# Optimization experiments

Hardware: AMD Instinct MI355X
Metric: run time of the kernel (lower is better)

Reference implementation:

```python
import jax, jax.numpy as jnp
import numpy as np

B, N, E = 32, 4096, 65536          # batch, num_agents(nodes), edges per graph
DS, ES, ENC, H, OUT = 8, 4, 8, 16, 4  # node state, edge state, encoding, hidden, out_state
NI = N * DS                        # flat obs size for critic


def setup_inputs() -> dict:
    key = jax.random.key(0)
    ks = jax.random.split(key, 18)
    g = lambda k, s: jax.random.normal(k, s, dtype=jnp.float32) * 0.1
    return {
        "agent_obs": jax.random.normal(ks[0], (B, N, DS), dtype=jnp.float32),
        "edge_attr": jax.random.normal(ks[1], (B, E, ES), dtype=jnp.float32),
        "obs_flat": jax.random.normal(ks[2], (B, NI), dtype=jnp.float32),
        "edge_index": jax.random.randint(ks[3], (B, 2, E), 0, N, dtype=jnp.int64),
        "W_ne1": g(ks[4], (DS, H)), "b_ne1": g(ks[5], (H,)),
        "W_ne2": g(ks[6], (H, ENC)), "b_ne2": g(ks[7], (ENC,)),
        "W_ee": g(ks[8], (ES, ENC)), "b_ee": g(ks[9], (ENC,)),
        "W_a1": g(ks[10], (ENC, H)), "b_a1": g(ks[11], (H,)),
        "W_a2": g(ks[12], (H, OUT)), "b_a2": g(ks[13], (OUT,)),
        "W_c1": g(ks[14], (NI, H)), "b_c1": g(ks[15], (H,)),
        "W_c2": g(ks[16], (H, 1)), "b_c2": g(ks[17], (1,)),
    }


def reference(agent_obs, edge_attr, obs_flat, edge_index,
              W_ne1, b_ne1, W_ne2, b_ne2, W_ee, b_ee,
              W_a1, b_a1, W_a2, b_a2, W_c1, b_c1, W_c2, b_c2):
    # node encoder: [B,N,DS] -> [B,N,ENC]
    x = jax.nn.relu(agent_obs @ W_ne1 + b_ne1) @ W_ne2 + b_ne2
    # edge encoder: [B,E,ES] -> [B,E,ENC]
    ea = edge_attr @ W_ee + b_ee
    src = edge_index[:, 0, :]  # [B,E] message source (x_j)
    dst = edge_index[:, 1, :]  # [B,E] aggregation target (x_i)
    # GINEConv message: relu(x_j + edge_attr)
    xj = jnp.take_along_axis(x, src[..., None], axis=1)  # [B,E,ENC]
    msgs = jax.nn.relu(xj + ea)
    # sum-aggregate to targets (batched via segment offsets)
    seg = (dst + jnp.arange(B, dtype=dst.dtype)[:, None] * N).reshape(-1)
    agg = jax.ops.segment_sum(msgs.reshape(B * E, ENC), seg, num_segments=B * N)
    agg = agg.reshape(B, N, ENC)
    # GINEConv nn (eps=0): MLP((1+eps)*x + agg)
    h = jax.nn.relu((x + agg) @ W_a1 + b_a1) @ W_a2 + b_a2  # [B,N,OUT]
    # per-sample flatten, drop first agent's out slots
    outs = h.reshape(B, N * OUT)[:, OUT:]  # [B,(N-1)*OUT]
    # critic on flat obs
    values = jax.nn.relu(obs_flat @ W_c1 + b_c1) @ W_c2 + b_c2  # [B,1]
    return jnp.concatenate([outs, values], axis=-1)  # [B,(N-1)*OUT+1]
```

## Files before the change

### kernel.cpp

```cpp
#include <hip/hip_runtime.h>
#include <hip/hip_fp16.h>

#define BB 32
#define NN 4096
#define EE 65536
#define DS 8
#define ES 4
#define ENC 8
#define HH 16
#define OUTC 4
#define NI (NN * DS)
#define ROW (NN * OUTC - OUTC + 1)
#define CSPLIT 16
#define CCHUNK (NI / CSPLIT)
#define ESPLIT 8
#define EPB (EE / ESPLIT)

typedef __fp16 half2_t __attribute__((ext_vector_type(2)));

__global__ __launch_bounds__(256) void k_fusedA(
    const float* __restrict__ obs,
    const float* __restrict__ Wne1, const float* __restrict__ bne1,
    const float* __restrict__ Wne2, const float* __restrict__ bne2,
    const float* __restrict__ obsf, const float* __restrict__ Wc1,
    float* __restrict__ x, float* __restrict__ hpart) {
  __shared__ float sW1[DS * HH], sb1[HH], sW2[HH * ENC], sb2[ENC];
  __shared__ float red[4][HH];
  int t = threadIdx.x;

  if (blockIdx.x < 512) {
    if (t < DS * HH)  sW1[t] = Wne1[t];
    if (t < HH)       sb1[t] = bne1[t];
    if (t < HH * ENC) sW2[t] = Wne2[t];
    if (t < ENC)      sb2[t] = bne2[t];
    __syncthreads();
    int gid = blockIdx.x * 256 + t;

    const float4* op = (const float4*)(obs + (size_t)gid * DS);
    float4 o0 = op[0], o1 = op[1];
    float o[DS] = {o0.x, o0.y, o0.z, o0.w, o1.x, o1.y, o1.z, o1.w};

    float hb[HH];
#pragma unroll
    for (int j = 0; j < HH; ++j) {
      float a = sb1[j];
#pragma unroll
      for (int i = 0; i < DS; ++i) a += o[i] * sW1[i * HH + j];
      hb[j] = fmaxf(a, 0.f);
    }
    float e[ENC];
#pragma unroll
    for (int c = 0; c < ENC; ++c) {
      float a = sb2[c];
#pragma unroll
      for (int j = 0; j < HH; ++j) a += hb[j] * sW2[j * ENC + c];
      e[c] = a;
    }
    float4* xp = (float4*)(x + (size_t)gid * ENC);
    xp[0] = make_float4(e[0], e[1], e[2], e[3]);
    xp[1] = make_float4(e[4], e[5], e[6], e[7]);
  } else {
    int cb = blockIdx.x - 512;
    int b = cb / CSPLIT, s = cb % CSPLIT;
    float acc[HH];
#pragma unroll
    for (int j = 0; j < HH; ++j) acc[j] = 0.f;

    const float* ob = obsf + (size_t)b * NI;
    int i0 = s * CCHUNK;
    for (int i = i0 + t; i < i0 + CCHUNK; i += 256) {
      float v = ob[i];
      const float4* wr = (const float4*)(Wc1 + (size_t)i * HH);
      float4 w0 = wr[0], w1 = wr[1], w2 = wr[2], w3 = wr[3];
      acc[0]  += v * w0.x; acc[1]  += v * w0.y; acc[2]  += v * w0.z; acc[3]  += v * w0.w;
      acc[4]  += v * w1.x; acc[5]  += v * w1.y; acc[6]  += v * w1.z; acc[7]  += v * w1.w;
      acc[8]  += v * w2.x; acc[9]  += v * w2.y; acc[10] += v * w2.z; acc[11] += v * w2.w;
      acc[12] += v * w3.x; acc[13] += v * w3.y; acc[14] += v * w3.z; acc[15] += v * w3.w;
    }
    int wid = t >> 6, lane = t & 63;
#pragma unroll
    for (int j = 0; j < HH; ++j) {
      float a = acc[j];
#pragma unroll
      for (int off = 32; off >= 1; off >>= 1) a += __shfl_down(a, off, 64);
      if (lane == 0) red[wid][j] = a;
    }
    __syncthreads();
    if (t < HH)
      hpart[(size_t)cb * HH + t] = red[0][t] + red[1][t] + red[2][t] + red[3][t];
  }
}

__global__ __launch_bounds__(1024, 4) void k_edge_full(
    const float* __restrict__ eattr,
    const int* __restrict__ eidx,
    const float* __restrict__ Wee, const float* __restrict__ bee,
    const float* __restrict__ x,
    float* __restrict__ partial) {
  __shared__ uint32_t sagg[4 * NN];
  int p = blockIdx.x;
  int L = (p & 7) * 32 + (p >> 3);
  int b = L >> 3, s = L & 7;
  int t = threadIdx.x;

  float wv[ES * ENC], bv[ENC];
#pragma unroll
  for (int i = 0; i < ES * ENC; ++i) wv[i] = Wee[i];
#pragma unroll
  for (int c = 0; c < ENC; ++c) bv[c] = bee[c];

  {
    uint4 z = make_uint4(0u, 0u, 0u, 0u);
    uint4* sz = (uint4*)sagg;
#pragma unroll
    for (int i = 0; i < (4 * NN / 4) / 1024; ++i) sz[t + i * 1024] = z;
  }
  __syncthreads();

  const int*    ibs = eidx + (size_t)b * 2 * EE + (size_t)s * EPB;
  const int*    ibd = ibs + EE;
  const float4* ab4 = (const float4*)eattr + (size_t)b * EE + (size_t)s * EPB;
  const float4* xb4 = (const float4*)(x + (size_t)b * NN * ENC);

#pragma unroll
  for (int uo = 0; uo < EPB / 4096; ++uo) {
    int k = t + uo * 4096;
    int s_[4], d_[4];
    float4 a_[4];
#pragma unroll
    for (int u = 0; u < 4; ++u) { s_[u] = ibs[k + u * 1024]; d_[u] = ibd[k + u * 1024]; }
#pragma unroll
    for (int u = 0; u < 4; ++u) a_[u] = ab4[k + u * 1024];
    float4 xl[4], xh[4];
#pragma unroll
    for (int u = 0; u < 4; ++u) { xl[u] = xb4[2 * s_[u]]; xh[u] = xb4[2 * s_[u] + 1]; }
#pragma unroll
    for (int u = 0; u < 4; ++u) {
      float av[ES] = {a_[u].x, a_[u].y, a_[u].z, a_[u].w};
      float xv[ENC] = {xl[u].x, xl[u].y, xl[u].z, xl[u].w,
                       xh[u].x, xh[u].y, xh[u].z, xh[u].w};
      float m[ENC];
#pragma unroll
      for (int c = 0; c < ENC; ++c) {
        float ea = bv[c];
#pragma unroll
        for (int i2 = 0; i2 < ES; ++i2) ea += av[i2] * wv[i2 * ENC + c];
        m[c] = fmaxf(xv[c] + ea, 0.f);
      }
      uint32_t base = (uint32_t)(uintptr_t)(&sagg[d_[u]]);
#pragma unroll
      for (int cp = 0; cp < 4; ++cp) {
        half2_t pk = __builtin_amdgcn_cvt_pkrtz(m[2 * cp], m[2 * cp + 1]);
        uint32_t pku = __builtin_bit_cast(uint32_t, pk);
        uint32_t addr = base + (uint32_t)(cp * NN * 4);
        asm volatile("ds_pk_add_f16 %0, %1" :: "v"(addr), "v"(pku) : "memory");
      }
    }
  }
  __syncthreads();

  float* pb = partial + (size_t)L * NN * ENC;
#pragma unroll
  for (int i = 0; i < NN / 1024; ++i) {
    int n = t + i * 1024;
    uint32_t w0 = sagg[0 * NN + n], w1 = sagg[1 * NN + n];
    uint32_t w2 = sagg[2 * NN + n], w3 = sagg[3 * NN + n];
    half2_t h0 = __builtin_bit_cast(half2_t, w0);
    half2_t h1 = __builtin_bit_cast(half2_t, w1);
    half2_t h2 = __builtin_bit_cast(half2_t, w2);
    half2_t h3 = __builtin_bit_cast(half2_t, w3);
    float4 lo = make_float4((float)h0[0], (float)h0[1], (float)h1[0], (float)h1[1]);
    float4 hi = make_float4((float)h2[0], (float)h2[1], (float)h3[0], (float)h3[1]);
    float4* dp = (float4*)(pb + (size_t)n * ENC);
    dp[0] = lo; dp[1] = hi;
  }
}

__global__ __launch_bounds__(256) void k_fusedC(
    const float* __restrict__ x, const float* __restrict__ partial,
    const float* __restrict__ Wa1, const float* __restrict__ ba1,
    const float* __restrict__ Wa2, const float* __restrict__ ba2,
    const float* __restrict__ hpart,
    const float* __restrict__ bc1,
    const float* __restrict__ Wc2, const float* __restrict__ bc2,
    float* __restrict__ out) {
  int t = threadIdx.x;
  if (blockIdx.x == 512) {
    if (t < BB) {
      int b = t;
      float val = bc2[0];
#pragma unroll
      for (int j = 0; j < HH; ++j) {
        float h = bc1[j];
        for (int s = 0; s < CSPLIT; ++s) h += hpart[(size_t)(b * CSPLIT + s) * HH + j];
        val += fmaxf(h, 0.f) * Wc2[j];
      }
      out[(size_t)b * ROW + (ROW - 1)] = val;
    }
    return;
  }
  __shared__ float sW1[ENC * HH], sb1[HH], sW2[HH * OUTC], sb2[OUTC];
  if (t < ENC * HH)  sW1[t] = Wa1[t];
  if (t < HH)        sb1[t] = ba1[t];
  if (t < HH * OUTC) sW2[t] = Wa2[t];
  if (t < OUTC)      sb2[t] = ba2[t];
  __syncthreads();
  int gid = blockIdx.x * 256 + t;
  int b = gid >> 12;
  int n = gid & (NN - 1);

  const float4* xp = (const float4*)(x + (size_t)gid * ENC);
  float4 xa = xp[0], xbv = xp[1];
  float4 aa = make_float4(0.f, 0.f, 0.f, 0.f), ab2 = aa;
  const float* pb = partial + ((size_t)(b * ESPLIT) * NN + n) * ENC;
#pragma unroll
  for (int s = 0; s < ESPLIT; ++s) {
    const float4* pp = (const float4*)(pb + (size_t)s * NN * ENC);
    float4 lo = pp[0], hi = pp[1];
    aa.x += lo.x; aa.y += lo.y; aa.z += lo.z; aa.w += lo.w;
    ab2.x += hi.x; ab2.y += hi.y; ab2.z += hi.z; ab2.w += hi.w;
  }
  float v[ENC] = {xa.x + aa.x, xa.y + aa.y, xa.z + aa.z, xa.w + aa.w,
                  xbv.x + ab2.x, xbv.y + ab2.y, xbv.z + ab2.z, xbv.w + ab2.w};

  float hb[HH];
#pragma unroll
  for (int j = 0; j < HH; ++j) {
    float a = sb1[j];
#pragma unroll
    for (int i = 0; i < ENC; ++i) a += v[i] * sW1[i * HH + j];
    hb[j] = fmaxf(a, 0.f);
  }
  float o[OUTC];
#pragma unroll
  for (int c = 0; c < OUTC; ++c) {
    float a = sb2[c];
#pragma unroll
    for (int j = 0; j < HH; ++j) a += hb[j] * sW2[j * OUTC + c];
    o[c] = a;
  }
  if (n > 0) {
    float* op = out + (size_t)b * ROW + (size_t)(n - 1) * OUTC;
    op[0] = o[0]; op[1] = o[1]; op[2] = o[2]; op[3] = o[3];
  }
}

extern "C" void kernel_launch(void* const* d_in, const int* in_sizes, int n_in,
                              void* d_out, int out_size, void* d_ws, size_t ws_size,
                              hipStream_t stream) {
  const float* agent_obs  = (const float*)d_in[0];
  const float* edge_attr  = (const float*)d_in[1];
  const float* obs_flat   = (const float*)d_in[2];
  const int*   edge_index = (const int*)d_in[3];
  const float* W_ne1 = (const float*)d_in[4];
  const float* b_ne1 = (const float*)d_in[5];
  const float* W_ne2 = (const float*)d_in[6];
  const float* b_ne2 = (const float*)d_in[7];
  const float* W_ee  = (const float*)d_in[8];
  const float* b_ee  = (const float*)d_in[9];
  const float* W_a1  = (const float*)d_in[10];
  const float* b_a1  = (const float*)d_in[11];
  const float* W_a2  = (const float*)d_in[12];
  const float* b_a2  = (const float*)d_in[13];
  const float* W_c1  = (const float*)d_in[14];
  const float* b_c1  = (const float*)d_in[15];
  const float* W_c2  = (const float*)d_in[16];
  const float* b_c2  = (const float*)d_in[17];
  float* out = (float*)d_out;

  float* x_buf   = (float*)d_ws;
  float* partial = x_buf + (size_t)BB * NN * ENC;
  float* hpart   = partial + (size_t)BB * ESPLIT * NN * ENC;

  k_fusedA<<<dim3(1024), dim3(256), 0, stream>>>(
      agent_obs, W_ne1, b_ne1, W_ne2, b_ne2, obs_flat, W_c1, x_buf, hpart);
  k_edge_full<<<dim3(BB * ESPLIT), dim3(1024), 0, stream>>>(
      edge_attr, edge_index, W_ee, b_ee, x_buf, partial);
  k_fusedC<<<dim3(513), dim3(256), 0, stream>>>(
      x_buf, partial, W_a1, b_a1, W_a2, b_a2, hpart, b_c1, W_c2, b_c2, out);
}
```

Before: 183.0 us.

## Fuse node encoder, edge scatter and critic partials into one mega kernel

Merges the node-encoder/critic kernel into the edge-aggregation kernel. Each block recomputes the node encoding for its whole graph into LDS as packed fp16, then gathers x_j from LDS instead of global memory. Warps 8-15 of each block compute critic partial dot products while warps 0-7 handle edges. This removes one launch and the global round trip for x, and stores x to global in fp16 for the tail kernel. In exchange, node encoding is done redundantly 8x per graph, LDS usage rises, and x loses precision.

```diff
diff --git a/kernel.cpp b/kernel.cpp
--- a/kernel.cpp
+++ b/kernel.cpp
@@ -11,157 +11,158 @@
 #define OUTC 4
 #define NI (NN * DS)
 #define ROW (NN * OUTC - OUTC + 1)
-#define CSPLIT 16
-#define CCHUNK (NI / CSPLIT)
 #define ESPLIT 8
 #define EPB (EE / ESPLIT)
+#define CUNITS (BB * 64)
 
 typedef __fp16 half2_t __attribute__((ext_vector_type(2)));
 
-__global__ __launch_bounds__(256) void k_fusedA(
+__global__ __launch_bounds__(1024, 4) void k_mega(
     const float* __restrict__ obs,
     const float* __restrict__ Wne1, const float* __restrict__ bne1,
     const float* __restrict__ Wne2, const float* __restrict__ bne2,
+    const float* __restrict__ eattr,
+    const int* __restrict__ eidx,
+    const float* __restrict__ Wee, const float* __restrict__ bee,
     const float* __restrict__ obsf, const float* __restrict__ Wc1,
-    float* __restrict__ x, float* __restrict__ hpart) {
-  __shared__ float sW1[DS * HH], sb1[HH], sW2[HH * ENC], sb2[ENC];
-  __shared__ float red[4][HH];
+    float* __restrict__ partial,
+    uint32_t* __restrict__ xg,
+    float* __restrict__ hpart) {
+  __shared__ uint32_t xl[NN * 4];
+  __shared__ uint32_t sagg[4 * NN];
+  __shared__ float sWn1[DS * HH], sbn1[HH], sWn2[HH * ENC], sbn2[ENC];
+
+  int p = blockIdx.x;
+  int L = (p & 7) * 32 + (p >> 3);
+  int b = L >> 3, s = L & 7;
   int t = threadIdx.x;
-
-  if (blockIdx.x < 512) {
-    if (t < DS * HH)  sW1[t] = Wne1[t];
-    if (t < HH)       sb1[t] = bne1[t];
-    if (t < HH * ENC) sW2[t] = Wne2[t];
-    if (t < ENC)      sb2[t] = bne2[t];
-    __syncthreads();
-    int gid = blockIdx.x * 256 + t;
-
-    const float4* op = (const float4*)(obs + (size_t)gid * DS);
+  int wv = t >> 6, lane = t & 63;
+
+  if (t < DS * HH)  sWn1[t] = Wne1[t];
+  if (t < HH)       sbn1[t] = bne1[t];
+  if (t < HH * ENC) sWn2[t] = Wne2[t];
+  if (t < ENC)      sbn2[t] = bne2[t];
+  {
+    uint4 z = make_uint4(0u, 0u, 0u, 0u);
+    uint4* sz = (uint4*)sagg;
+#pragma unroll
+    for (int i = 0; i < 4; ++i) sz[t + i * 1024] = z;
+  }
+  __syncthreads();
+
+#pragma unroll
+  for (int i = 0; i < 4; ++i) {
+    int n = t + i * 1024;
+    const float4* op = (const float4*)(obs + ((size_t)b * NN + n) * DS);
     float4 o0 = op[0], o1 = op[1];
     float o[DS] = {o0.x, o0.y, o0.z, o0.w, o1.x, o1.y, o1.z, o1.w};
-
     float hb[HH];
 #pragma unroll
     for (int j = 0; j < HH; ++j) {
-      float a = sb1[j];
-#pragma unroll
-      for (int i = 0; i < DS; ++i) a += o[i] * sW1[i * HH + j];
+      float a = sbn1[j];
+#pragma unroll
+      for (int k2 = 0; k2 < DS; ++k2) a += o[k2] * sWn1[k2 * HH + j];
       hb[j] = fmaxf(a, 0.f);
     }
     float e[ENC];
 #pragma unroll
     for (int c = 0; c < ENC; ++c) {
-      float a = sb2[c];
-#pragma unroll
-      for (int j = 0; j < HH; ++j) a += hb[j] * sW2[j * ENC + c];
+      float a = sbn2[c];
+#pragma unroll
+      for (int j = 0; j < HH; ++j) a += hb[j] * sWn2[j * ENC + c];
       e[c] = a;
     }
-    float4* xp = (float4*)(x + (size_t)gid * ENC);
-    xp[0] = make_float4(e[0], e[1], e[2], e[3]);
-    xp[1] = make_float4(e[4], e[5], e[6], e[7]);
+    uint4 pk;
+    pk.x = __builtin_bit_cast(uint32_t, __builtin_amdgcn_cvt_pkrtz(e[0], e[1]));
+    pk.y = __builtin_bit_cast(uint32_t, __builtin_amdgcn_cvt_pkrtz(e[2], e[3]));
+    pk.z = __builtin_bit_cast(uint32_t, __builtin_amdgcn_cvt_pkrtz(e[4], e[5]));
+    pk.w = __builtin_bit_cast(uint32_t, __builtin_amdgcn_cvt_pkrtz(e[6], e[7]));
+    *(uint4*)(&xl[n * 4]) = pk;
+  }
+  __syncthreads();
+
+  if (wv < 8) {
+    float wvv[ES * ENC], bvv[ENC];
+#pragma unroll
+    for (int i = 0; i < ES * ENC; ++i) wvv[i] = Wee[i];
+#pragma unroll
+    for (int c = 0; c < ENC; ++c) bvv[c] = bee[c];
+
+    const int*    ibs = eidx + (size_t)b * 2 * EE + (size_t)s * EPB + wv * 1024;
+    const int*    ibd = ibs + EE;
+    const float4* ab4 = (const float4*)eattr + (size_t)b * EE + (size_t)s * EPB + wv * 1024;
+
+#pragma unroll
+    for (int g = 0; g < 4; ++g) {
+      int s_[4], d_[4];
+      float4 a_[4];
+#pragma unroll
+      for (int u = 0; u < 4; ++u) {
+        int k = g * 256 + u * 64 + lane;
+        s_[u] = ibs[k]; d_[u] = ibd[k];
+      }
+#pragma unroll
+      for (int u = 0; u < 4; ++u) a_[u] = ab4[g * 256 + u * 64 + lane];
+      uint4 xp_[4];
+#pragma unroll
+      for (int u = 0; u < 4; ++u) xp_[u] = *(const uint4*)(&xl[s_[u] * 4]);
+#pragma unroll
+      for (int u = 0; u < 4; ++u) {
+        half2_t h0 = __builtin_bit_cast(half2_t, xp_[u].x);
+        half2_t h1 = __builtin_bit_cast(half2_t, xp_[u].y);
+        half2_t h2 = __builtin_bit_cast(half2_t, xp_[u].z);
+        half2_t h3 = __builtin_bit_cast(half2_t, xp_[u].w);
+        float xv[ENC] = {(float)h0[0], (float)h0[1], (float)h1[0], (float)h1[1],
+                         (float)h2[0], (float)h2[1], (float)h3[0], (float)h3[1]};
+        float av[ES] = {a_[u].x, a_[u].y, a_[u].z, a_[u].w};
+        float m[ENC];
+#pragma unroll
+        for (int c = 0; c < ENC; ++c) {
+          float ea = bvv[c];
+#pragma unroll
+          for (int i2 = 0; i2 < ES; ++i2) ea += av[i2] * wvv[i2 * ENC + c];
+          m[c] = fmaxf(xv[c] + ea, 0.f);
+        }
+        uint32_t base = (uint32_t)(uintptr_t)(&sagg[d_[u]]);
+#pragma unroll
+        for (int cp = 0; cp < 4; ++cp) {
+          half2_t pk = __builtin_amdgcn_cvt_pkrtz(m[2 * cp], m[2 * cp + 1]);
+          uint32_t pku = __builtin_bit_cast(uint32_t, pk);
+          uint32_t addr = base + (uint32_t)(cp * NN * 4);
+          asm volatile("ds_pk_add_f16 %0, %1" :: "v"(addr), "v"(pku) : "memory");
+        }
+      }
+    }
   } else {
-    int cb = blockIdx.x - 512;
-    int b = cb / CSPLIT, s = cb % CSPLIT;
+    int uw = p * 8 + (wv - 8);
+    int cb = uw >> 6, q = uw & 63;
+    const float* ob = obsf + (size_t)cb * NI;
     float acc[HH];
 #pragma unroll
     for (int j = 0; j < HH; ++j) acc[j] = 0.f;
-
-    const float* ob = obsf + (size_t)b * NI;
-    int i0 = s * CCHUNK;
-    for (int i = i0 + t; i < i0 + CCHUNK; i += 256) {
-      float v = ob[i];
-      const float4* wr = (const float4*)(Wc1 + (size_t)i * HH);
+#pragma unroll
+    for (int i = 0; i < 8; ++i) {
+      int r = q * 512 + i * 64 + lane;
+      float v = ob[r];
+      const float4* wr = (const float4*)(Wc1 + (size_t)r * HH);
       float4 w0 = wr[0], w1 = wr[1], w2 = wr[2], w3 = wr[3];
       acc[0]  += v * w0.x; acc[1]  += v * w0.y; acc[2]  += v * w0.z; acc[3]  += v * w0.w;
       acc[4]  += v * w1.x; acc[5]  += v * w1.y; acc[6]  += v * w1.z; acc[7]  += v * w1.w;
       acc[8]  += v * w2.x; acc[9]  += v * w2.y; acc[10] += v * w2.z; acc[11] += v * w2.w;
       acc[12] += v * w3.x; acc[13] += v * w3.y; acc[14] += v * w3.z; acc[15] += v * w3.w;
     }
-    int wid = t >> 6, lane = t & 63;
 #pragma unroll
     for (int j = 0; j < HH; ++j) {
-      float a = acc[j];
-#pragma unroll
-      for (int off = 32; off >= 1; off >>= 1) a += __shfl_down(a, off, 64);
-      if (lane == 0) red[wid][j] = a;
-    }
-    __syncthreads();
-    if (t < HH)
-      hpart[(size_t)cb * HH + t] = red[0][t] + red[1][t] + red[2][t] + red[3][t];
-  }
-}
-
-__global__ __launch_bounds__(1024, 4) void k_edge_full(
-    const float* __restrict__ eattr,
-    const int* __restrict__ eidx,
-    const float* __restrict__ Wee, const float* __restrict__ bee,
-    const float* __restrict__ x,
-    float* __restrict__ partial) {
-  __shared__ uint32_t sagg[4 * NN];
-  int p = blockIdx.x;
-  int L = (p & 7) * 32 + (p >> 3);
-  int b = L >> 3, s = L & 7;
-  int t = threadIdx.x;
-
-  float wv[ES * ENC], bv[ENC];
-#pragma unroll
-  for (int i = 0; i < ES * ENC; ++i) wv[i] = Wee[i];
-#pragma unroll
-  for (int c = 0; c < ENC; ++c) bv[c] = bee[c];
-
-  {
-    uint4 z = make_uint4(0u, 0u, 0u, 0u);
-    uint4* sz = (uint4*)sagg;
-#pragma unroll
-    for (int i = 0; i < (4 * NN / 4) / 1024; ++i) sz[t + i * 1024] = z;
-  }
-  __syncthreads();
-
-  const int*    ibs = eidx + (size_t)b * 2 * EE + (size_t)s * EPB;
-  const int*    ibd = ibs + EE;
-  const float4* ab4 = (const float4*)eattr + (size_t)b * EE + (size_t)s * EPB;
-  const float4* xb4 = (const float4*)(x + (size_t)b * NN * ENC);
-
-#pragma unroll
-  for (int uo = 0; uo < EPB / 4096; ++uo) {
-    int k = t + uo * 4096;
-    int s_[4], d_[4];
-    float4 a_[4];
-#pragma unroll
-    for (int u = 0; u < 4; ++u) { s_[u] = ibs[k + u * 1024]; d_[u] = ibd[k + u * 1024]; }
-#pragma unroll
-    for (int u = 0; u < 4; ++u) a_[u] = ab4[k + u * 1024];
-    float4 xl[4], xh[4];
-#pragma unroll
-    for (int u = 0; u < 4; ++u) { xl[u] = xb4[2 * s_[u]]; xh[u] = xb4[2 * s_[u] + 1]; }
-#pragma unroll
-    for (int u = 0; u < 4; ++u) {
-      float av[ES] = {a_[u].x, a_[u].y, a_[u].z, a_[u].w};
-      float xv[ENC] = {xl[u].x, xl[u].y, xl[u].z, xl[u].w,
-                       xh[u].x, xh[u].y, xh[u].z, xh[u].w};
-      float m[ENC];
-#pragma unroll
-      for (int c = 0; c < ENC; ++c) {
-        float ea = bv[c];
-#pragma unroll
-        for (int i2 = 0; i2 < ES; ++i2) ea += av[i2] * wv[i2 * ENC + c];
-        m[c] = fmaxf(xv[c] + ea, 0.f);
-      }
-      uint32_t base = (uint32_t)(uintptr_t)(&sagg[d_[u]]);
-#pragma unroll
-      for (int cp = 0; cp < 4; ++cp) {
-        half2_t pk = __builtin_amdgcn_cvt_pkrtz(m[2 * cp], m[2 * cp + 1]);
-        uint32_t pku = __builtin_bit_cast(uint32_t, pk);
-        uint32_t addr = base + (uint32_t)(cp * NN * 4);
-        asm volatile("ds_pk_add_f16 %0, %1" :: "v"(addr), "v"(pku) : "memory");
-      }
-    }
+#pragma unroll
+      for (int mres = 1; mres < 64; mres <<= 1) acc[j] += __shfl_xor(acc[j], mres, 64);
+    }
+    if (lane < HH) hpart[(size_t)uw * HH + lane] = acc[lane];
   }
   __syncthreads();
 
   float* pb = partial + (size_t)L * NN * ENC;
 #pragma unroll
-  for (int i = 0; i < NN / 1024; ++i) {
+  for (int i = 0; i < 4; ++i) {
     int n = t + i * 1024;
     uint32_t w0 = sagg[0 * NN + n], w1 = sagg[1 * NN + n];
     uint32_t w2 = sagg[2 * NN + n], w3 = sagg[3 * NN + n];
@@ -174,10 +175,18 @@
     float4* dp = (float4*)(pb + (size_t)n * ENC);
     dp[0] = lo; dp[1] = hi;
   }
+  if (s == 0) {
+    uint4* xg4 = (uint4*)xg + (size_t)b * NN;
+#pragma unroll
+    for (int i = 0; i < 4; ++i) {
+      int n = t + i * 1024;
+      xg4[n] = *(uint4*)(&xl[n * 4]);
+    }
+  }
 }
 
-__global__ __launch_bounds__(256) void k_fusedC(
-    const float* __restrict__ x, const float* __restrict__ partial,
+__global__ __launch_bounds__(256) void k_tail(
+    const uint32_t* __restrict__ xg, const float* __restrict__ partial,
     const float* __restrict__ Wa1, const float* __restrict__ ba1,
     const float* __restrict__ Wa2, const float* __restrict__ ba2,
     const float* __restrict__ hpart,
@@ -188,13 +197,17 @@
   if (blockIdx.x == 512) {
     if (t < BB) {
       int b = t;
+      float hsum[HH];
+#pragma unroll
+      for (int j = 0; j < HH; ++j) hsum[j] = bc1[j];
+      for (int u = 0; u < 64; ++u) {
+        const float* hp = hpart + (size_t)(b * 64 + u) * HH;
+#pragma unroll
+        for (int j = 0; j < HH; ++j) hsum[j] += hp[j];
+      }
       float val = bc2[0];
 #pragma unroll
-      for (int j = 0; j < HH; ++j) {
-        float h = bc1[j];
-        for (int s = 0; s < CSPLIT; ++s) h += hpart[(size_t)(b * CSPLIT + s) * HH + j];
-        val += fmaxf(h, 0.f) * Wc2[j];
-      }
+      for (int j = 0; j < HH; ++j) val += fmaxf(hsum[j], 0.f) * Wc2[j];
       out[(size_t)b * ROW + (ROW - 1)] = val;
     }
     return;
@@ -209,19 +222,21 @@
   int b = gid >> 12;
   int n = gid & (NN - 1);
 
-  const float4* xp = (const float4*)(x + (size_t)gid * ENC);
-  float4 xa = xp[0], xbv = xp[1];
-  float4 aa = make_float4(0.f, 0.f, 0.f, 0.f), ab2 = aa;
+  uint4 xp = ((const uint4*)xg)[gid];
+  half2_t x0 = __builtin_bit_cast(half2_t, xp.x);
+  half2_t x1 = __builtin_bit_cast(half2_t, xp.y);
+  half2_t x2 = __builtin_bit_cast(half2_t, xp.z);
+  half2_t x3 = __builtin_bit_cast(half2_t, xp.w);
+  float v[ENC] = {(float)x0[0], (float)x0[1], (float)x1[0], (float)x1[1],
+                  (float)x2[0], (float)x2[1], (float)x3[0], (float)x3[1]};
   const float* pb = partial + ((size_t)(b * ESPLIT) * NN + n) * ENC;
 #pragma unroll
   for (int s = 0; s < ESPLIT; ++s) {
     const float4* pp = (const float4*)(pb + (size_t)s * NN * ENC);
     float4 lo = pp[0], hi = pp[1];
-    aa.x += lo.x; aa.y += lo.y; aa.z += lo.z; aa.w += lo.w;
-    ab2.x += hi.x; ab2.y += hi.y; ab2.z += hi.z; ab2.w += hi.w;
-  }
-  float v[ENC] = {xa.x + aa.x, xa.y + aa.y, xa.z + aa.z, xa.w + aa.w,
-                  xbv.x + ab2.x, xbv.y + ab2.y, xbv.z + ab2.z, xbv.w + ab2.w};
+    v[0] += lo.x; v[1] += lo.y; v[2] += lo.z; v[3] += lo.w;
+    v[4] += hi.x; v[5] += hi.y; v[6] += hi.z; v[7] += hi.w;
+  }
 
   float hb[HH];
 #pragma unroll
@@ -268,14 +283,14 @@
   const float* b_c2  = (const float*)d_in[17];
   float* out = (float*)d_out;
 
-  float* x_buf   = (float*)d_ws;
-  float* partial = x_buf + (size_t)BB * NN * ENC;
-  float* hpart   = partial + (size_t)BB * ESPLIT * NN * ENC;
-
-  k_fusedA<<<dim3(1024), dim3(256), 0, stream>>>(
-      agent_obs, W_ne1, b_ne1, W_ne2, b_ne2, obs_flat, W_c1, x_buf, hpart);
-  k_edge_full<<<dim3(BB * ESPLIT), dim3(1024), 0, stream>>>(
-      edge_attr, edge_index, W_ee, b_ee, x_buf, partial);
-  k_fusedC<<<dim3(513), dim3(256), 0, stream>>>(
-      x_buf, partial, W_a1, b_a1, W_a2, b_a2, hpart, b_c1, W_c2, b_c2, out);
+  float*    partial = (float*)d_ws;
+  uint32_t* xg      = (uint32_t*)(partial + (size_t)BB * ESPLIT * NN * ENC);
+  float*    hpart   = (float*)(xg + (size_t)BB * NN * 4);
+
+  k_mega<<<dim3(BB * ESPLIT), dim3(1024), 0, stream>>>(
+      agent_obs, W_ne1, b_ne1, W_ne2, b_ne2,
+      edge_attr, edge_index, W_ee, b_ee,
+      obs_flat, W_c1, partial, xg, hpart);
+  k_tail<<<dim3(513), dim3(256), 0, stream>>>(
+      xg, partial, W_a1, b_a1, W_a2, b_a2, hpart, b_c1, W_c2, b_c2, out);
 }
```

Result: slower. 376.5 us (+105.8%).
